# Kernel optimization log

Hardware: AMD Instinct MI355X
Metric: run time of the kernel (lower is better)

## Reference

```python
import jax, jax.numpy as jnp
import numpy as np

B, T, I, H = 256, 512, 256, 512


def setup_inputs() -> dict:
    key = jax.random.key(0)
    ks = jax.random.split(key, 7)
    s_ih = 1.0 / np.sqrt(I)
    s_hh = 1.0 / np.sqrt(H)
    return {
        "x": jax.random.normal(ks[0], (B, T, I), dtype=jnp.float32),
        "w_ih": jax.random.uniform(ks[1], (3 * H, I), jnp.float32, -s_ih, s_ih),
        "w_hh": jax.random.uniform(ks[2], (3 * H, H), jnp.float32, -s_hh, s_hh),
        "b": jax.random.uniform(ks[3], (3 * H,), jnp.float32, -s_hh, s_hh),
        "b_n": jax.random.uniform(ks[4], (H,), jnp.float32, -s_hh, s_hh),
        "w_proj": jax.random.uniform(ks[5], (1, H), jnp.float32, -s_hh, s_hh),
        "b_proj": jax.random.uniform(ks[6], (1,), jnp.float32, -s_hh, s_hh),
    }


def reference(x, w_ih, w_hh, b, b_n, w_proj, b_proj):
    # x: (B, T, I). Precompute all input-gate projections in one big GEMM.
    Bb, Tt, _ = x.shape
    Hh = w_hh.shape[1]
    igates = jnp.einsum("bti,gi->tbg", x, w_ih) + b  # (T, B, 3H)
    ir, iz, inn = jnp.split(igates, 3, axis=-1)  # each (T, B, H)

    def step(h, ig):
        ir_t, iz_t, in_t = ig
        hg = h @ w_hh.T  # (B, 3H)
        hr, hz, hn = jnp.split(hg, 3, axis=-1)
        r = jax.nn.sigmoid(ir_t + hr)
        z = jax.nn.sigmoid(iz_t + hz)
        n = jnp.tanh(in_t + r * (hn + b_n))
        # equinox GRUCell update: new + z * (hidden - new)
        h_new = n + z * (h - n)
        return h_new, None

    h0 = jnp.zeros((Bb, Hh), dtype=x.dtype)
    hT, _ = jax.lax.scan(step, h0, (ir, iz, inn))  # (B, H)
    e = hT @ w_proj.T + b_proj  # (B, 1)
    return jnp.squeeze(e, axis=-1)  # (B,)
```

## Files before the change

### kernel.cpp

```cpp
#include <hip/hip_runtime.h>
#include <stdint.h>

#define B_  256
#define T_  512
#define I_  256
#define H_  512
#define G3_ 1536

typedef _Float16 half8  __attribute__((ext_vector_type(8)));
typedef _Float16 half4v __attribute__((ext_vector_type(4)));
typedef __fp16   fp16x2 __attribute__((ext_vector_type(2)));
typedef float    float4v __attribute__((ext_vector_type(4)));

__device__ __forceinline__ float sigmoid_f(float x) { return 1.f / (1.f + __expf(-x)); }
__device__ __forceinline__ float tanh_f(float x) {
  x = fminf(15.f, fmaxf(-15.f, x));
  float e = __expf(2.f * x);
  return (e - 1.f) / (e + 1.f);
}

__device__ __forceinline__ unsigned pk2(float lo, float hi) {
  fp16x2 p = __builtin_amdgcn_cvt_pkrtz(lo, hi);
  return *(unsigned*)&p;
}

__global__ __launch_bounds__(256) void igates_gemm(
    const float* __restrict__ x, const float* __restrict__ w_ih,
    const float* __restrict__ bias, _Float16* __restrict__ ig)
{
  __shared__ _Float16 Ash[128][72];
  __shared__ _Float16 Bsh[128][72];
  const int tid  = threadIdx.x;
  const int lane = tid & 63;
  const int wv   = tid >> 6;
  const int wm   = wv >> 1, wn = wv & 1;
  const int n0   = blockIdx.x * 128;
  const int m0   = blockIdx.y * 128;
  const int cn   = lane & 15;
  const int rq   = lane >> 4;

  float4v acc[4][4];
  #pragma unroll
  for (int a = 0; a < 4; ++a)
    #pragma unroll
    for (int c = 0; c < 4; ++c) acc[a][c] = (float4v){0.f, 0.f, 0.f, 0.f};

  for (int kc = 0; kc < I_; kc += 64) {
    #pragma unroll
    for (int i = 0; i < 8; ++i) {
      int e   = tid + (i << 8);
      int row = e >> 4;
      int c4  = e & 15;
      int m   = m0 + row;
      int tt  = m >> 8, bb = m & 255;
      float4 va = *(const float4*)(x + ((size_t)bb * T_ + tt) * I_ + kc + (c4 << 2));
      uint2 ua; ua.x = pk2(va.x, va.y); ua.y = pk2(va.z, va.w);
      *(uint2*)&Ash[row][c4 << 2] = ua;
      float4 vb = *(const float4*)(w_ih + (size_t)(n0 + row) * I_ + kc + (c4 << 2));
      uint2 ub; ub.x = pk2(vb.x, vb.y); ub.y = pk2(vb.z, vb.w);
      *(uint2*)&Bsh[row][c4 << 2] = ub;
    }
    __syncthreads();
    #pragma unroll
    for (int ks = 0; ks < 2; ++ks) {
      int kk = (ks << 5) + (rq << 3);
      half8 af[4], bf[4];
      #pragma unroll
      for (int mt = 0; mt < 4; ++mt)
        af[mt] = *(const half8*)&Ash[(wm << 6) + (mt << 4) + cn][kk];
      #pragma unroll
      for (int nt = 0; nt < 4; ++nt)
        bf[nt] = *(const half8*)&Bsh[(wn << 6) + (nt << 4) + cn][kk];
      #pragma unroll
      for (int mt = 0; mt < 4; ++mt)
        #pragma unroll
        for (int nt = 0; nt < 4; ++nt)
          acc[mt][nt] = __builtin_amdgcn_mfma_f32_16x16x32_f16(af[mt], bf[nt], acc[mt][nt], 0, 0, 0);
    }
    __syncthreads();
  }
  float bv[4];
  #pragma unroll
  for (int nt = 0; nt < 4; ++nt) bv[nt] = bias[n0 + (wn << 6) + (nt << 4) + cn];
  #pragma unroll
  for (int mt = 0; mt < 4; ++mt)
    #pragma unroll
    for (int nt = 0; nt < 4; ++nt) {
      int mrow = m0 + (wm << 6) + (mt << 4) + (rq << 2);
      int ncol = n0 + (wn << 6) + (nt << 4) + cn;
      #pragma unroll
      for (int r = 0; r < 4; ++r)
        ig[(size_t)(mrow + r) * G3_ + ncol] = (_Float16)(acc[mt][nt][r] + bv[nt]);
    }
}

__global__ __launch_bounds__(256, 1) void gru_scan(
    const _Float16* __restrict__ ig, const float* __restrict__ w_hh,
    const float* __restrict__ b_n,
    uint32_t* __restrict__ hb0, uint32_t* __restrict__ hb1)
{
  __shared__ _Float16 h_lds[16][520];

  const int tid  = threadIdx.x;
  const int lane = tid & 63;
  const int wv   = tid >> 6;
  const int blk  = blockIdx.x;
  const int gb   = ((blk & 7) << 1) | ((blk >> 3) & 1);
  const int gs   = blk >> 4;
  const int b0   = gb << 4;
  const int j0   = gs << 6;
  const int jw   = j0 + (wv << 4);
  const int cn   = lane & 15;
  const int rq   = lane >> 4;

  half8 wfrag[3][16];
  #pragma unroll
  for (int g = 0; g < 3; ++g) {
    const float* wrow = w_hh + (size_t)(g * H_ + jw + cn) * H_;
    #pragma unroll
    for (int ks = 0; ks < 16; ++ks) {
      int k = (ks << 5) + (rq << 3);
      half8 w;
      #pragma unroll
      for (int i = 0; i < 8; ++i) w[i] = (_Float16)wrow[k + i];
      wfrag[g][ks] = w;
    }
  }
  const float bnv = b_n[jw + cn];

  uint32_t* bufs[2] = { hb0, hb1 };

  for (int t = 0; t < T_; ++t) {
    const uint64_t* src = (const uint64_t*)bufs[t & 1] + ((size_t)b0 << 8);
    uint64_t hv[16];
    #pragma unroll
    for (int i = 0; i < 16; ++i)
      hv[i] = __hip_atomic_load(src + (i << 8) + tid,
                                __ATOMIC_RELAXED, __HIP_MEMORY_SCOPE_AGENT);

    float igv[3][4];
    {
      const _Float16* igb =
          ig + (size_t)(t * B_ + b0 + (rq << 2)) * G3_ + jw + cn;
      #pragma unroll
      for (int g = 0; g < 3; ++g)
        #pragma unroll
        for (int r = 0; r < 4; ++r)
          igv[g][r] = (float)igb[(size_t)r * G3_ + g * H_];
    }

    const uint64_t patt = ((uint64_t)(uint32_t)t << 16) | ((uint64_t)(uint32_t)t << 48);
    uint32_t pend = 0;
    #pragma unroll
    for (int i = 0; i < 16; ++i)
      if ((hv[i] & 0xFFFF0000FFFF0000ULL) != patt) pend |= (1u << i);
    while (pend) {
      #pragma unroll
      for (int i = 0; i < 16; ++i)
        if (pend & (1u << i))
          hv[i] = __hip_atomic_load(src + (i << 8) + tid,
                                    __ATOMIC_RELAXED, __HIP_MEMORY_SCOPE_AGENT);
      #pragma unroll
      for (int i = 0; i < 16; ++i)
        if ((pend & (1u << i)) && (hv[i] & 0xFFFF0000FFFF0000ULL) == patt)
          pend &= ~(1u << i);
    }

    #pragma unroll
    for (int i = 0; i < 16; ++i) {
      int idx = (i << 8) + tid;
      int row = idx >> 8, cp = idx & 255;
      uint32_t pk = (uint32_t)(hv[i] & 0xFFFF) | ((uint32_t)(hv[i] >> 32) << 16);
      *(uint32_t*)&h_lds[row][cp << 1] = pk;
    }
    __syncthreads();

    float4v acc[3][2];
    #pragma unroll
    for (int g = 0; g < 3; ++g) {
      acc[g][0] = (float4v){0.f, 0.f, 0.f, 0.f};
      acc[g][1] = (float4v){0.f, 0.f, 0.f, 0.f};
    }
    #pragma unroll
    for (int ks = 0; ks < 16; ++ks) {
      half8 a = *(const half8*)&h_lds[cn][(ks << 5) + (rq << 3)];
      int p = ks & 1;
      acc[0][p] = __builtin_amdgcn_mfma_f32_16x16x32_f16(a, wfrag[0][ks], acc[0][p], 0, 0, 0);
      acc[1][p] = __builtin_amdgcn_mfma_f32_16x16x32_f16(a, wfrag[1][ks], acc[1][p], 0, 0, 0);
      acc[2][p] = __builtin_amdgcn_mfma_f32_16x16x32_f16(a, wfrag[2][ks], acc[2][p], 0, 0, 0);
    }

    uint32_t* dst = bufs[(t + 1) & 1];
    const uint32_t tagbits = (uint32_t)(t + 1) << 16;
    #pragma unroll
    for (int r = 0; r < 4; ++r) {
      float rg = sigmoid_f(igv[0][r] + acc[0][0][r] + acc[0][1][r]);
      float zg = sigmoid_f(igv[1][r] + acc[1][0][r] + acc[1][1][r]);
      float nv = tanh_f(igv[2][r] + rg * (acc[2][0][r] + acc[2][1][r] + bnv));
      float hp = (float)h_lds[(rq << 2) + r][jw + cn];
      _Float16 hh = (_Float16)(nv + zg * (hp - nv));
      uint32_t val = tagbits | (uint32_t)*(uint16_t*)&hh;
      __hip_atomic_store(dst + (((size_t)(b0 + (rq << 2) + r)) << 9) + jw + cn,
                         val, __ATOMIC_RELAXED, __HIP_MEMORY_SCOPE_AGENT);
    }
    __syncthreads();
  }
}

__global__ __launch_bounds__(64) void proj_kernel(
    const uint32_t* __restrict__ h, const float* __restrict__ w_proj,
    const float* __restrict__ b_proj, float* __restrict__ out)
{
  int b = blockIdx.x;
  int lane = threadIdx.x;
  float s = 0.f;
  #pragma unroll
  for (int i = 0; i < 8; ++i) {
    int j = lane + (i << 6);
    uint16_t u = (uint16_t)(h[((size_t)b << 9) + j] & 0xFFFF);
    s += (float)*(_Float16*)&u * w_proj[j];
  }
  #pragma unroll
  for (int off = 32; off > 0; off >>= 1) s += __shfl_down(s, off, 64);
  if (lane == 0) out[b] = s + b_proj[0];
}

extern "C" void kernel_launch(void* const* d_in, const int* in_sizes, int n_in,
                              void* d_out, int out_size, void* d_ws, size_t ws_size,
                              hipStream_t stream) {
  const float* x      = (const float*)d_in[0];
  const float* w_ih   = (const float*)d_in[1];
  const float* w_hh   = (const float*)d_in[2];
  const float* bias   = (const float*)d_in[3];
  const float* b_n    = (const float*)d_in[4];
  const float* w_proj = (const float*)d_in[5];
  const float* b_proj = (const float*)d_in[6];
  float* out = (float*)d_out;

  char* ws = (char*)d_ws;
  const size_t IG_BYTES = (size_t)T_ * B_ * G3_ * sizeof(_Float16);
  const size_t HB_BYTES = (size_t)B_ * H_ * sizeof(uint32_t);
  _Float16* igbuf = (_Float16*)ws;
  uint32_t* hbuf0 = (uint32_t*)(ws + IG_BYTES);
  uint32_t* hbuf1 = (uint32_t*)(ws + IG_BYTES + HB_BYTES);

  (void)hipMemsetAsync(ws + IG_BYTES, 0, HB_BYTES, stream);

  dim3 gridA(G3_ / 128, (T_ * B_) / 128);
  igates_gemm<<<gridA, 256, 0, stream>>>(x, w_ih, bias, igbuf);
  gru_scan<<<128, 256, 0, stream>>>(igbuf, w_hh, b_n, hbuf0, hbuf1);
  proj_kernel<<<B_, 64, 0, stream>>>(hbuf0, w_proj, b_proj, out);
}
```

Before: 2.563 ms.

## Interleave two batch chains per block and replace tagged h with flag sync

```diff
diff --git a/kernel.cpp b/kernel.cpp
--- a/kernel.cpp
+++ b/kernel.cpp
@@ -8,7 +8,6 @@
 #define G3_ 1536
 
 typedef _Float16 half8  __attribute__((ext_vector_type(8)));
-typedef _Float16 half4v __attribute__((ext_vector_type(4)));
 typedef __fp16   fp16x2 __attribute__((ext_vector_type(2)));
 typedef float    float4v __attribute__((ext_vector_type(4)));
 
@@ -22,6 +21,17 @@
 __device__ __forceinline__ unsigned pk2(float lo, float hi) {
   fp16x2 p = __builtin_amdgcn_cvt_pkrtz(lo, hi);
   return *(unsigned*)&p;
+}
+
+__device__ __forceinline__ uint32_t min8_u64x4(const uint64_t f[4]) {
+  uint32_t m = 0xFFFFFFFFu;
+  #pragma unroll
+  for (int k = 0; k < 4; ++k) {
+    uint32_t lo = (uint32_t)f[k], hi = (uint32_t)(f[k] >> 32);
+    m = m < lo ? m : lo;
+    m = m < hi ? m : hi;
+  }
+  return m;
 }
 
 __global__ __launch_bounds__(256) void igates_gemm(
@@ -97,21 +107,23 @@
 __global__ __launch_bounds__(256, 1) void gru_scan(
     const _Float16* __restrict__ ig, const float* __restrict__ w_hh,
     const float* __restrict__ b_n,
-    uint32_t* __restrict__ hb0, uint32_t* __restrict__ hb1)
+    _Float16* __restrict__ hb0, _Float16* __restrict__ hb1,
+    int* flags)
 {
   __shared__ _Float16 h_lds[16][520];
+  __shared__ _Float16 hn_lds[16][72];
 
   const int tid  = threadIdx.x;
   const int lane = tid & 63;
   const int wv   = tid >> 6;
   const int blk  = blockIdx.x;
-  const int gb   = ((blk & 7) << 1) | ((blk >> 3) & 1);
-  const int gs   = blk >> 4;
-  const int b0   = gb << 4;
+  const int q    = blk & 7;
+  const int gs   = blk >> 3;
   const int j0   = gs << 6;
   const int jw   = j0 + (wv << 4);
   const int cn   = lane & 15;
   const int rq   = lane >> 4;
+  const int chain0 = q << 1;
 
   half8 wfrag[3][16];
   #pragma unroll
@@ -128,87 +140,122 @@
   }
   const float bnv = b_n[jw + cn];
 
-  uint32_t* bufs[2] = { hb0, hb1 };
-
-  for (int t = 0; t < T_; ++t) {
-    const uint64_t* src = (const uint64_t*)bufs[t & 1] + ((size_t)b0 << 8);
-    uint64_t hv[16];
-    #pragma unroll
-    for (int i = 0; i < 16; ++i)
-      hv[i] = __hip_atomic_load(src + (i << 8) + tid,
-                                __ATOMIC_RELAXED, __HIP_MEMORY_SCOPE_AGENT);
-
-    float igv[3][4];
-    {
-      const _Float16* igb =
-          ig + (size_t)(t * B_ + b0 + (rq << 2)) * G3_ + jw + cn;
-      #pragma unroll
-      for (int g = 0; g < 3; ++g)
+  _Float16* bufs[2] = { hb0, hb1 };
+
+  uint64_t fpre[2][4];
+  float igv[2][3][4];
+
+  {
+    const _Float16* igb = ig + (size_t)((chain0 << 4) + (rq << 2)) * G3_ + jw + cn;
+    #pragma unroll
+    for (int g = 0; g < 3; ++g)
+      #pragma unroll
+      for (int r4 = 0; r4 < 4; ++r4)
+        igv[0][g][r4] = (float)igb[(size_t)r4 * G3_ + g * H_];
+  }
+
+  for (int r = 0; r < T_; ++r) {
+    #pragma unroll
+    for (int s = 0; s < 2; ++s) {
+      const int chain = chain0 | s;
+      const int b0    = chain << 4;
+
+      uint32_t mn = 0;
+      if (r > 0) {
+        mn = min8_u64x4(fpre[s]);
+        if (mn < (uint32_t)r) {
+          const uint64_t* fp = (const uint64_t*)(flags + (chain << 3));
+          uint64_t f[4];
+          do {
+            #pragma unroll
+            for (int k = 0; k < 4; ++k)
+              f[k] = __hip_atomic_load(fp + k, __ATOMIC_RELAXED,
+                                       __HIP_MEMORY_SCOPE_AGENT);
+            mn = min8_u64x4(f);
+          } while (mn < (uint32_t)r);
+        }
+      }
+
+      const uint64_t* src = (const uint64_t*)bufs[r & 1]
+                          + ((size_t)b0 << 7) + (mn >> 31);
+      uint64_t hv[8];
+      #pragma unroll
+      for (int i = 0; i < 8; ++i)
+        hv[i] = __hip_atomic_load(src + (i << 8) + tid,
+                                  __ATOMIC_RELAXED, __HIP_MEMORY_SCOPE_AGENT);
+
+      __builtin_amdgcn_s_waitcnt(0);
+
+      {
+        int fv = (s == 0) ? r : (r + 1);
+        if (!(s == 0 && r == 0) && tid == 0)
+          __hip_atomic_store(&flags[((chain ^ 1) << 3) | gs], fv,
+                             __ATOMIC_RELAXED, __HIP_MEMORY_SCOPE_AGENT);
+      }
+
+      #pragma unroll
+      for (int i = 0; i < 8; ++i) {
+        int idx = (i << 8) + tid;
+        int row = idx >> 7, c = idx & 127;
+        *(uint64_t*)&h_lds[row][c << 2] = hv[i];
+      }
+      __syncthreads();
+
+      float4v acc[3][2];
+      #pragma unroll
+      for (int g = 0; g < 3; ++g) {
+        acc[g][0] = (float4v){0.f, 0.f, 0.f, 0.f};
+        acc[g][1] = (float4v){0.f, 0.f, 0.f, 0.f};
+      }
+      #pragma unroll
+      for (int ks = 0; ks < 16; ++ks) {
+        half8 a = *(const half8*)&h_lds[cn][(ks << 5) + (rq << 3)];
+        int pp = ks & 1;
+        acc[0][pp] = __builtin_amdgcn_mfma_f32_16x16x32_f16(a, wfrag[0][ks], acc[0][pp], 0, 0, 0);
+        acc[1][pp] = __builtin_amdgcn_mfma_f32_16x16x32_f16(a, wfrag[1][ks], acc[1][pp], 0, 0, 0);
+        acc[2][pp] = __builtin_amdgcn_mfma_f32_16x16x32_f16(a, wfrag[2][ks], acc[2][pp], 0, 0, 0);
+      }
+      #pragma unroll
+      for (int r4 = 0; r4 < 4; ++r4) {
+        float rg = sigmoid_f(igv[s][0][r4] + acc[0][0][r4] + acc[0][1][r4]);
+        float zg = sigmoid_f(igv[s][1][r4] + acc[1][0][r4] + acc[1][1][r4]);
+        float nv = tanh_f(igv[s][2][r4] + rg * (acc[2][0][r4] + acc[2][1][r4] + bnv));
+        float hp = (float)h_lds[(rq << 2) + r4][jw + cn];
+        hn_lds[(rq << 2) + r4][(wv << 4) + cn] = (_Float16)(nv + zg * (hp - nv));
+      }
+      __syncthreads();
+
+      {
+        int row = tid >> 4, c = tid & 15;
+        uint64_t v = *(const uint64_t*)&hn_lds[row][c << 2];
+        __hip_atomic_store((uint64_t*)bufs[(r + 1) & 1]
+                               + ((size_t)(b0 + row) << 7) + (gs << 4) + c,
+                           v, __ATOMIC_RELAXED, __HIP_MEMORY_SCOPE_AGENT);
+      }
+
+      {
+        const uint64_t* fpn = (const uint64_t*)(flags + ((chain ^ 1) << 3));
         #pragma unroll
-        for (int r = 0; r < 4; ++r)
-          igv[g][r] = (float)igb[(size_t)r * G3_ + g * H_];
-    }
-
-    const uint64_t patt = ((uint64_t)(uint32_t)t << 16) | ((uint64_t)(uint32_t)t << 48);
-    uint32_t pend = 0;
-    #pragma unroll
-    for (int i = 0; i < 16; ++i)
-      if ((hv[i] & 0xFFFF0000FFFF0000ULL) != patt) pend |= (1u << i);
-    while (pend) {
-      #pragma unroll
-      for (int i = 0; i < 16; ++i)
-        if (pend & (1u << i))
-          hv[i] = __hip_atomic_load(src + (i << 8) + tid,
-                                    __ATOMIC_RELAXED, __HIP_MEMORY_SCOPE_AGENT);
-      #pragma unroll
-      for (int i = 0; i < 16; ++i)
-        if ((pend & (1u << i)) && (hv[i] & 0xFFFF0000FFFF0000ULL) == patt)
-          pend &= ~(1u << i);
-    }
-
-    #pragma unroll
-    for (int i = 0; i < 16; ++i) {
-      int idx = (i << 8) + tid;
-      int row = idx >> 8, cp = idx & 255;
-      uint32_t pk = (uint32_t)(hv[i] & 0xFFFF) | ((uint32_t)(hv[i] >> 32) << 16);
-      *(uint32_t*)&h_lds[row][cp << 1] = pk;
-    }
-    __syncthreads();
-
-    float4v acc[3][2];
-    #pragma unroll
-    for (int g = 0; g < 3; ++g) {
-      acc[g][0] = (float4v){0.f, 0.f, 0.f, 0.f};
-      acc[g][1] = (float4v){0.f, 0.f, 0.f, 0.f};
-    }
-    #pragma unroll
-    for (int ks = 0; ks < 16; ++ks) {
-      half8 a = *(const half8*)&h_lds[cn][(ks << 5) + (rq << 3)];
-      int p = ks & 1;
-      acc[0][p] = __builtin_amdgcn_mfma_f32_16x16x32_f16(a, wfrag[0][ks], acc[0][p], 0, 0, 0);
-      acc[1][p] = __builtin_amdgcn_mfma_f32_16x16x32_f16(a, wfrag[1][ks], acc[1][p], 0, 0, 0);
-      acc[2][p] = __builtin_amdgcn_mfma_f32_16x16x32_f16(a, wfrag[2][ks], acc[2][p], 0, 0, 0);
-    }
-
-    uint32_t* dst = bufs[(t + 1) & 1];
-    const uint32_t tagbits = (uint32_t)(t + 1) << 16;
-    #pragma unroll
-    for (int r = 0; r < 4; ++r) {
-      float rg = sigmoid_f(igv[0][r] + acc[0][0][r] + acc[0][1][r]);
-      float zg = sigmoid_f(igv[1][r] + acc[1][0][r] + acc[1][1][r]);
-      float nv = tanh_f(igv[2][r] + rg * (acc[2][0][r] + acc[2][1][r] + bnv));
-      float hp = (float)h_lds[(rq << 2) + r][jw + cn];
-      _Float16 hh = (_Float16)(nv + zg * (hp - nv));
-      uint32_t val = tagbits | (uint32_t)*(uint16_t*)&hh;
-      __hip_atomic_store(dst + (((size_t)(b0 + (rq << 2) + r)) << 9) + jw + cn,
-                         val, __ATOMIC_RELAXED, __HIP_MEMORY_SCOPE_AGENT);
-    }
-    __syncthreads();
+        for (int k = 0; k < 4; ++k)
+          fpre[s ^ 1][k] = __hip_atomic_load(fpn + k, __ATOMIC_RELAXED,
+                                             __HIP_MEMORY_SCOPE_AGENT);
+      }
+      {
+        int tn = (s == 0) ? r : (r + 1 < T_ ? r + 1 : T_ - 1);
+        const _Float16* igb = ig
+            + (size_t)(tn * B_ + ((chain ^ 1) << 4) + (rq << 2)) * G3_ + jw + cn;
+        #pragma unroll
+        for (int g = 0; g < 3; ++g)
+          #pragma unroll
+          for (int r4 = 0; r4 < 4; ++r4)
+            igv[s ^ 1][g][r4] = (float)igb[(size_t)r4 * G3_ + g * H_];
+      }
+    }
   }
 }
 
 __global__ __launch_bounds__(64) void proj_kernel(
-    const uint32_t* __restrict__ h, const float* __restrict__ w_proj,
+    const _Float16* __restrict__ h, const float* __restrict__ w_proj,
     const float* __restrict__ b_proj, float* __restrict__ out)
 {
   int b = blockIdx.x;
@@ -217,8 +264,7 @@
   #pragma unroll
   for (int i = 0; i < 8; ++i) {
     int j = lane + (i << 6);
-    uint16_t u = (uint16_t)(h[((size_t)b << 9) + j] & 0xFFFF);
-    s += (float)*(_Float16*)&u * w_proj[j];
+    s += (float)h[((size_t)b << 9) + j] * w_proj[j];
   }
   #pragma unroll
   for (int off = 32; off > 0; off >>= 1) s += __shfl_down(s, off, 64);
@@ -239,15 +285,16 @@
 
   char* ws = (char*)d_ws;
   const size_t IG_BYTES = (size_t)T_ * B_ * G3_ * sizeof(_Float16);
-  const size_t HB_BYTES = (size_t)B_ * H_ * sizeof(uint32_t);
+  const size_t HB_BYTES = (size_t)B_ * H_ * sizeof(_Float16);
   _Float16* igbuf = (_Float16*)ws;
-  uint32_t* hbuf0 = (uint32_t*)(ws + IG_BYTES);
-  uint32_t* hbuf1 = (uint32_t*)(ws + IG_BYTES + HB_BYTES);
-
-  (void)hipMemsetAsync(ws + IG_BYTES, 0, HB_BYTES, stream);
+  _Float16* hbuf0 = (_Float16*)(ws + IG_BYTES);
+  _Float16* hbuf1 = (_Float16*)(ws + IG_BYTES + HB_BYTES);
+  int*      flags = (int*)(ws + IG_BYTES + 2 * HB_BYTES);
+
+  (void)hipMemsetAsync(ws + IG_BYTES, 0, 2 * HB_BYTES + 1024, stream);
 
   dim3 gridA(G3_ / 128, (T_ * B_) / 128);
   igates_gemm<<<gridA, 256, 0, stream>>>(x, w_ih, bias, igbuf);
-  gru_scan<<<128, 256, 0, stream>>>(igbuf, w_hh, b_n, hbuf0, hbuf1);
+  gru_scan<<<64, 256, 0, stream>>>(igbuf, w_hh, b_n, hbuf0, hbuf1, flags);
   proj_kernel<<<B_, 64, 0, stream>>>(hbuf0, w_proj, b_proj, out);
 }
```

Measured after the change: 3.060 ms. 1.19x slower.
